# Optimization experiments

Measured on AMD Instinct MI355X. Metric: run time of the kernel, lower is better.

Reference implementation:

```python
import jax, jax.numpy as jnp
import numpy as np
from jax import lax

IMG, P, L, H, D, MLPD, NC, B = 224, 16, 12, 12, 768, 3072, 1000, 32
G = IMG // P          # 14 patches per side
S = G * G + 1         # 197 tokens (class token + patches)
DH = D // H           # 64 head dim
EPS = 1e-6


def setup_inputs() -> dict:
    key = jax.random.key(0)
    ks = jax.random.split(key, 10)
    def nrm(k, shape, s=0.02):
        return jax.random.normal(k, shape, jnp.float32) * s
    return {
        "x": jax.random.normal(ks[0], (B, 3, IMG, IMG), jnp.float32),
        "tangent": jax.random.normal(ks[1], (B, 3, IMG, IMG), jnp.float32),
        "conv_w": nrm(ks[2], (D, 3, P, P)),
        "conv_b": jnp.zeros((D,), jnp.float32),
        "class_token": jnp.zeros((1, 1, D), jnp.float32),
        "pos_emb": nrm(ks[3], (1, S, D)),
        "ln1_g": jnp.ones((L, D), jnp.float32), "ln1_b": jnp.zeros((L, D), jnp.float32),
        "qkv_w": nrm(ks[4], (L, 3 * D, D)), "qkv_b": jnp.zeros((L, 3 * D), jnp.float32),
        "out_w": nrm(ks[5], (L, D, D)), "out_b": jnp.zeros((L, D), jnp.float32),
        "ln2_g": jnp.ones((L, D), jnp.float32), "ln2_b": jnp.zeros((L, D), jnp.float32),
        "fc1_w": nrm(ks[6], (L, MLPD, D)), "fc1_b": jnp.zeros((L, MLPD), jnp.float32),
        "fc2_w": nrm(ks[7], (L, D, MLPD)), "fc2_b": jnp.zeros((L, D), jnp.float32),
        "lnf_g": jnp.ones((D,), jnp.float32), "lnf_b": jnp.zeros((D,), jnp.float32),
        "head_w": nrm(ks[8], (NC, D)), "head_b": jnp.zeros((NC,), jnp.float32),
    }


def _layer_norm(x, g, b):
    mu = jnp.mean(x, -1, keepdims=True)
    var = jnp.mean(jnp.square(x - mu), -1, keepdims=True)
    return (x - mu) * lax.rsqrt(var + EPS) * g + b


def _vit(x, conv_w, conv_b, class_token, pos_emb, ln1_g, ln1_b, qkv_w, qkv_b,
         out_w, out_b, ln2_g, ln2_b, fc1_w, fc1_b, fc2_w, fc2_b, lnf_g, lnf_b,
         head_w, head_b):
    n = x.shape[0]
    # patch embedding == Conv2d(3, D, kernel=P, stride=P)
    xr = x.reshape(n, 3, G, P, G, P)
    tok = jnp.einsum('ncgphq,dcpq->nghd', xr, conv_w).reshape(n, G * G, D) + conv_b
    cls = jnp.broadcast_to(class_token, (n, 1, D))
    z = jnp.concatenate([cls, tok], axis=1) + pos_emb  # [n, S, D]

    def block(z, p):
        l1g, l1b, qw, qb, ow, ob, l2g, l2b, f1w, f1b, f2w, f2b = p
        y = _layer_norm(z, l1g, l1b)
        qkv = jnp.einsum('nsd,ed->nse', y, qw) + qb          # [n,S,3D]
        q, k, v = jnp.split(qkv, 3, axis=-1)
        q = q.reshape(n, S, H, DH).transpose(0, 2, 1, 3)
        k = k.reshape(n, S, H, DH).transpose(0, 2, 1, 3)
        v = v.reshape(n, S, H, DH).transpose(0, 2, 1, 3)
        scores = jnp.einsum('nhqd,nhkd->nhqk', q, k) / jnp.sqrt(jnp.float32(DH))
        a = jax.nn.softmax(scores, axis=-1)
        o = jnp.einsum('nhqk,nhkd->nhqd', a, v).transpose(0, 2, 1, 3).reshape(n, S, D)
        o = jnp.einsum('nsd,ed->nse', o, ow) + ob
        z = z + o
        y2 = _layer_norm(z, l2g, l2b)
        h = jax.nn.gelu(jnp.einsum('nsd,ed->nse', y2, f1w) + f1b, approximate=False)
        z = z + jnp.einsum('nse,de->nsd', h, f2w) + f2b
        return z, None

    z, _ = lax.scan(block, z, (ln1_g, ln1_b, qkv_w, qkv_b, out_w, out_b,
                               ln2_g, ln2_b, fc1_w, fc1_b, fc2_w, fc2_b))
    z = _layer_norm(z, lnf_g, lnf_b)
    return z[:, 0] @ head_w.T + head_b  # [n, NC]


def reference(x, tangent, conv_w, conv_b, class_token, pos_emb, ln1_g, ln1_b,
              qkv_w, qkv_b, out_w, out_b, ln2_g, ln2_b, fc1_w, fc1_b, fc2_w,
              fc2_b, lnf_g, lnf_b, head_w, head_b):
    f = lambda xx: _vit(xx, conv_w, conv_b, class_token, pos_emb, ln1_g, ln1_b,
                        qkv_w, qkv_b, out_w, out_b, ln2_g, ln2_b, fc1_w, fc1_b,
                        fc2_w, fc2_b, lnf_g, lnf_b, head_w, head_b)
    out, out_jvp = jax.jvp(f, (x,), (tangent,))
    return out, out_jvp
```

## Files before the change

### kernel.cpp

```cpp
#include <hip/hip_runtime.h>
#include <math.h>

static constexpr int B_   = 32;
static constexpr int S_   = 197;
static constexpr int D_   = 768;
static constexpr int H_   = 12;
static constexpr int L_   = 12;
static constexpr int MD_  = 3072;
static constexpr int NC_  = 1000;
static constexpr int GP_  = 196;
static constexpr int KP_  = 224;
static constexpr int MP_  = 6400;

typedef __attribute__((ext_vector_type(8))) short bf16x8v;
typedef __attribute__((ext_vector_type(4))) float f32x4v;

__device__ __forceinline__ unsigned short f2bf(float x) {
    union { float f; unsigned u; } v; v.f = x;
    unsigned r = v.u + 0x7fffu + ((v.u >> 16) & 1u);
    return (unsigned short)(r >> 16);
}

#define GLOAD_LDS16(gptr, lptr) \
    __builtin_amdgcn_global_load_lds((const __attribute__((address_space(1))) void*)(gptr), \
        (__attribute__((address_space(3))) void*)(lptr), 16, 0, 0)

template<bool ACC, bool BIAS, bool OUTBF>
__global__ __launch_bounds__(512, 4) void mfma_gemm_kernel(
    const short* __restrict__ A, const short* __restrict__ Bm,
    const float* __restrict__ bias, void* __restrict__ Cv,
    int M, int N, int K, int ldc, int bias_rows)
{
    int bx, by;
    {
        const int gx = gridDim.x, nwg = gx * gridDim.y;
        const int flat = blockIdx.y * gx + blockIdx.x;
        const int q = nwg >> 3, r = nwg & 7;
        const int xcd = flat & 7, idx = flat >> 3;
        const int nf = (xcd < r ? xcd * (q + 1) : r * (q + 1) + (xcd - r) * q) + idx;
        bx = nf % gx; by = nf / gx;
    }
    __shared__ __align__(16) short ldsA[2][128 * 32];
    __shared__ __align__(16) short ldsB[2][128 * 32];
    const int tid  = threadIdx.x;
    const int lane = tid & 63;
    const int w    = tid >> 6;
    const int m0 = by * 128, n0 = bx * 128;
    const int wr = w >> 1, wc = w & 1;
    f32x4v acc[2][4] = {};

    const int r_in = lane >> 2;
    const int cdst = lane & 3;
    const int srow = w * 16 + r_in;
    const int csrc = cdst ^ ((srow >> 1) & 3);
    const size_t aoff = (size_t)(m0 + srow) * K + csrc * 8;
    const size_t boff = (size_t)(n0 + srow) * K + csrc * 8;

    GLOAD_LDS16(A  + aoff, &ldsA[0][w * 512]);
    GLOAD_LDS16(Bm + boff, &ldsB[0][w * 512]);
    __syncthreads();

    int cur = 0;
    for (int k0 = 0; k0 < K; k0 += 32) {
        const int nxt = cur ^ 1;
        if (k0 + 32 < K) {
            GLOAD_LDS16(A  + aoff + k0 + 32, &ldsA[nxt][w * 512]);
            GLOAD_LDS16(Bm + boff + k0 + 32, &ldsB[nxt][w * 512]);
        }
        const short* La = ldsA[cur];
        const short* Lb = ldsB[cur];
        bf16x8v af[2], bfr[4];
        #pragma unroll
        for (int m = 0; m < 2; ++m) {
            const int row = wr * 32 + m * 16 + (lane & 15);
            const int c = (lane >> 4) ^ ((row >> 1) & 3);
            af[m] = *(const bf16x8v*)&La[row * 32 + c * 8];
        }
        #pragma unroll
        for (int n = 0; n < 4; ++n) {
            const int row = wc * 64 + n * 16 + (lane & 15);
            const int c = (lane >> 4) ^ ((row >> 1) & 3);
            bfr[n] = *(const bf16x8v*)&Lb[row * 32 + c * 8];
        }
        #pragma unroll
        for (int m = 0; m < 2; ++m)
            #pragma unroll
            for (int n = 0; n < 4; ++n)
                acc[m][n] = __builtin_amdgcn_mfma_f32_16x16x32_bf16(af[m], bfr[n], acc[m][n], 0, 0, 0);
        __syncthreads();
        cur = nxt;
    }
    const int col_base = n0 + wc * 64 + (lane & 15);
    const int row_base = m0 + wr * 32 + (lane >> 4) * 4;
    #pragma unroll
    for (int n = 0; n < 4; ++n) {
        const int col = col_base + n * 16;
        const float bv = BIAS ? bias[col] : 0.f;
        #pragma unroll
        for (int m = 0; m < 2; ++m) {
            const int row = row_base + m * 16;
            const float bvr = (BIAS && row < bias_rows) ? bv : 0.f;
            #pragma unroll
            for (int r = 0; r < 4; ++r) {
                if (row + r < M) {
                    const size_t off = (size_t)(row + r) * ldc + col;
                    const float v = acc[m][n][r] + bvr;
                    if (OUTBF) ((short*)Cv)[off] = (short)f2bf(v);
                    else if (ACC) ((float*)Cv)[off] += v;
                    else ((float*)Cv)[off] = v;
                }
            }
        }
    }
}

__global__ __launch_bounds__(256) void attn_fused_kernel(
    const short* __restrict__ qkvb, const short* __restrict__ dqkvb,
    const short* __restrict__ Vtb_, const short* __restrict__ dVtb_,
    short* __restrict__ obf, short* __restrict__ dobf)
{
    const int qt = blockIdx.x;
    const int b  = blockIdx.y;
    const int n = b / H_, h = b - n * H_;
    const short* qb  = qkvb  + (size_t)n * S_ * 2304 + h * 64;
    const short* kb  = qb + 768;
    const short* dqb = dqkvb + (size_t)n * S_ * 2304 + h * 64;
    const short* dkb = dqb + 768;
    const short* Vb  = Vtb_  + (size_t)b * 64 * KP_;
    const short* dVb = dVtb_ + (size_t)b * 64 * KP_;

    __shared__ __align__(16) short lds[32768];
    const int tid = threadIdx.x, lane = tid & 63, w = tid >> 6;
    const int g = lane >> 4, kc = lane & 15;
    const int srow = lane >> 2, cdst = lane & 3;
    const int csrc = cdst ^ ((srow >> 1) & 3);

    {
        const size_t qr = (size_t)min(qt * 64 + w * 16 + srow, S_ - 1) * 2304;
        #pragma unroll
        for (int kw = 0; kw < 2; ++kw) {
            GLOAD_LDS16(qb  + qr + kw * 32 + csrc * 8, &lds[w * 1024 + kw * 512]);
            GLOAD_LDS16(dqb + qr + kw * 32 + csrc * 8, &lds[4096 + w * 1024 + kw * 512]);
        }
    }

    f32x4v aS[14], aD[14];
    #pragma unroll
    for (int i = 0; i < 14; ++i) { aS[i] = (f32x4v){0,0,0,0}; aD[i] = (f32x4v){0,0,0,0}; }
    bf16x8v qf[2], dqf[2];

    #pragma unroll
    for (int kt = 0; kt < 7; ++kt) {
        {
            const int kwin = w & 1;
            const short* src = (w < 2) ? kb : dkb;
            const int base = (w < 2) ? 8192 : 10240;
            #pragma unroll
            for (int half = 0; half < 2; ++half) {
                const size_t kr = (size_t)min(kt * 32 + half * 16 + srow, S_ - 1) * 2304;
                GLOAD_LDS16(src + kr + kwin * 32 + csrc * 8,
                            &lds[base + kwin * 1024 + half * 512]);
            }
        }
        __syncthreads();
        if (kt == 0) {
            #pragma unroll
            for (int kw = 0; kw < 2; ++kw) {
                const int c = g ^ ((kc >> 1) & 3);
                qf[kw]  = *(const bf16x8v*)&lds[w * 1024 + kw * 512 + kc * 32 + c * 8];
                dqf[kw] = *(const bf16x8v*)&lds[4096 + w * 1024 + kw * 512 + kc * 32 + c * 8];
            }
        }
        #pragma unroll
        for (int nf = 0; nf < 2; ++nf) {
            const int row = nf * 16 + kc;
            const int c = g ^ ((row >> 1) & 3);
            const bf16x8v kf0  = *(const bf16x8v*)&lds[8192  + row * 32 + c * 8];
            const bf16x8v kf1  = *(const bf16x8v*)&lds[8192  + 1024 + row * 32 + c * 8];
            const bf16x8v dkf0 = *(const bf16x8v*)&lds[10240 + row * 32 + c * 8];
            const bf16x8v dkf1 = *(const bf16x8v*)&lds[10240 + 1024 + row * 32 + c * 8];
            const int fi = kt * 2 + nf;
            aS[fi] = __builtin_amdgcn_mfma_f32_16x16x32_bf16(qf[0], kf0, aS[fi], 0,0,0);
            aS[fi] = __builtin_amdgcn_mfma_f32_16x16x32_bf16(qf[1], kf1, aS[fi], 0,0,0);
            aD[fi] = __builtin_amdgcn_mfma_f32_16x16x32_bf16(dqf[0], kf0, aD[fi], 0,0,0);
            aD[fi] = __builtin_amdgcn_mfma_f32_16x16x32_bf16(dqf[1], kf1, aD[fi], 0,0,0);
            aD[fi] = __builtin_amdgcn_mfma_f32_16x16x32_bf16(qf[0], dkf0, aD[fi], 0,0,0);
            aD[fi] = __builtin_amdgcn_mfma_f32_16x16x32_bf16(qf[1], dkf1, aD[fi], 0,0,0);
        }
        __syncthreads();
    }

    float pm[4] = {-3.0e38f, -3.0e38f, -3.0e38f, -3.0e38f};
    #pragma unroll
    for (int fi = 0; fi < 14; ++fi) {
        if (fi * 16 + kc < S_) {
            #pragma unroll
            for (int r = 0; r < 4; ++r) pm[r] = fmaxf(pm[r], aS[fi][r]);
        }
    }
    #pragma unroll
    for (int off = 1; off < 16; off <<= 1)
        #pragma unroll
        for (int r = 0; r < 4; ++r) pm[r] = fmaxf(pm[r], __shfl_xor(pm[r], off));

    float den[4] = {0,0,0,0}, tsm[4] = {0,0,0,0};
    #pragma unroll
    for (int fi = 0; fi < 14; ++fi) {
        const bool val = fi * 16 + kc < S_;
        #pragma unroll
        for (int r = 0; r < 4; ++r) {
            const float s  = aS[fi][r] * 0.125f;
            const float ds = aD[fi][r] * 0.125f;
            const float e = val ? expf(s - pm[r] * 0.125f) : 0.f;
            den[r] += e; tsm[r] += e * ds;
            aS[fi][r] = e; aD[fi][r] = ds;
        }
    }
    #pragma unroll
    for (int off = 1; off < 16; off <<= 1)
        #pragma unroll
        for (int r = 0; r < 4; ++r) {
            den[r] += __shfl_xor(den[r], off);
            tsm[r] += __shfl_xor(tsm[r], off);
        }
    float inv[4], tq[4];
    #pragma unroll
    for (int r = 0; r < 4; ++r) { inv[r] = 1.f / den[r]; tq[r] = tsm[r] * inv[r]; }

    const int lpw = w * 3584, ldpw = 14336 + w * 3584;
    #pragma unroll
    for (int fi = 0; fi < 14; ++fi) {
        const int kwin = fi >> 1;
        const int chunkbase = (fi & 1) * 2 + (kc >> 3);
        #pragma unroll
        for (int r = 0; r < 4; ++r) {
            const int qs = g * 4 + r;
            const int swz = chunkbase ^ ((qs >> 1) & 3);
            const int addr = kwin * 512 + qs * 32 + swz * 8 + (kc & 7);
            const float p  = aS[fi][r] * inv[r];
            const float dp = p * (aD[fi][r] - tq[r]);
            lds[lpw  + addr] = (short)f2bf(p);
            lds[ldpw + addr] = (short)f2bf(dp);
        }
    }

    f32x4v aO[4], aDO[4];
    #pragma unroll
    for (int i = 0; i < 4; ++i) { aO[i] = (f32x4v){0,0,0,0}; aDO[i] = (f32x4v){0,0,0,0}; }

    #pragma unroll
    for (int kt = 0; kt < 7; ++kt) {
        {
            const size_t vr = (size_t)(w * 16 + srow) * KP_ + kt * 32 + csrc * 8;
            GLOAD_LDS16(Vb  + vr, &lds[28672 + w * 512]);
            GLOAD_LDS16(dVb + vr, &lds[30720 + w * 512]);
        }
        __syncthreads();
        bf16x8v pa, dpa;
        {
            const int c = g ^ ((kc >> 1) & 3);
            pa  = *(const bf16x8v*)&lds[lpw  + kt * 512 + kc * 32 + c * 8];
            dpa = *(const bf16x8v*)&lds[ldpw + kt * 512 + kc * 32 + c * 8];
        }
        #pragma unroll
        for (int nf = 0; nf < 4; ++nf) {
            const int row = nf * 16 + kc;
            const int c = (g) ^ ((row >> 1) & 3);
            const bf16x8v vf  = *(const bf16x8v*)&lds[28672 + row * 32 + c * 8];
            const bf16x8v dvf = *(const bf16x8v*)&lds[30720 + row * 32 + c * 8];
            aO[nf]  = __builtin_amdgcn_mfma_f32_16x16x32_bf16(pa,  vf,  aO[nf], 0,0,0);
            aDO[nf] = __builtin_amdgcn_mfma_f32_16x16x32_bf16(dpa, vf,  aDO[nf], 0,0,0);
            aDO[nf] = __builtin_amdgcn_mfma_f32_16x16x32_bf16(pa,  dvf, aDO[nf], 0,0,0);
        }
        __syncthreads();
    }

    short* ob  = obf  + (size_t)n * S_ * D_ + h * 64;
    short* dob = dobf + (size_t)n * S_ * D_ + h * 64;
    #pragma unroll
    for (int nf = 0; nf < 4; ++nf) {
        const int dh = nf * 16 + kc;
        #pragma unroll
        for (int r = 0; r < 4; ++r) {
            const int q = qt * 64 + w * 16 + g * 4 + r;
            if (q < S_) {
                ob [(size_t)q * D_ + dh] = (short)f2bf(aO[nf][r]);
                dob[(size_t)q * D_ + dh] = (short)f2bf(aDO[nf][r]);
            }
        }
    }
}

__global__ __launch_bounds__(256) void vtrans_kernel(
    const short* __restrict__ qkvb, const short* __restrict__ dqkvb,
    short* __restrict__ Vt, short* __restrict__ dVt)
{
    const int blk = blockIdx.x;
    const int b = blk >> 2, kt = blk & 3;
    const int n = b / H_, h = b - n * H_;
    const short* vb  = qkvb  + (size_t)n * S_ * 2304 + 1536 + h * 64;
    const short* dvb = dqkvb + (size_t)n * S_ * 2304 + 1536 + h * 64;
    __shared__ short t1[64][65], t2[64][65];
    const int tid = threadIdx.x;
    #pragma unroll
    for (int j = 0; j < 16; ++j) {
        const int e = tid + 256 * j;
        const int kk = e >> 6, dh = e & 63;
        const int gk = kt * 64 + kk;
        short v = 0, dv = 0;
        if (gk < S_) { v = vb[(size_t)gk * 2304 + dh]; dv = dvb[(size_t)gk * 2304 + dh]; }
        t1[dh][kk] = v; t2[dh][kk] = dv;
    }
    __syncthreads();
    #pragma unroll
    for (int j = 0; j < 16; ++j) {
        const int e = tid + 256 * j;
        const int dh = e >> 6, kk = e & 63;
        const int ok = kt * 64 + kk;
        if (ok < KP_) {
            Vt [(size_t)b * 64 * KP_ + (size_t)dh * KP_ + ok] = t1[dh][kk];
            dVt[(size_t)b * 64 * KP_ + (size_t)dh * KP_ + ok] = t2[dh][kk];
        }
    }
}

template<bool BIAS>
__global__ __launch_bounds__(256) void gemm_kernel(
    const float* __restrict__ A, const float* __restrict__ Bm,
    const float* __restrict__ bias, float* __restrict__ C,
    int M, int N, int K, int lda, int ldb, int ldc)
{
    const int tile_m = blockIdx.y * 64, tile_n = blockIdx.x * 64;
    __shared__ float As[16][64];
    __shared__ float Bs[16][64];
    const int tid = threadIdx.x;
    const int tx = tid & 15, ty = tid >> 4;
    float acc[4][4] = {};
    for (int k0 = 0; k0 < K; k0 += 16) {
        {
            const int row = tid >> 2, kc = (tid & 3) * 4, gm = tile_m + row;
            #pragma unroll
            for (int i = 0; i < 4; ++i) {
                const int gk = k0 + kc + i;
                float v = 0.f;
                if (gm < M && gk < K) v = A[(long long)gm * lda + gk];
                As[kc + i][row] = v;
            }
        }
        {
            const int row = tid >> 2, kc = (tid & 3) * 4, gn = tile_n + row;
            #pragma unroll
            for (int i = 0; i < 4; ++i) {
                const int gk = k0 + kc + i;
                float v = 0.f;
                if (gn < N && gk < K) v = Bm[(long long)gn * ldb + gk];
                Bs[kc + i][row] = v;
            }
        }
        __syncthreads();
        #pragma unroll
        for (int kk = 0; kk < 16; ++kk) {
            float a[4], bb[4];
            #pragma unroll
            for (int i = 0; i < 4; ++i) a[i] = As[kk][ty * 4 + i];
            #pragma unroll
            for (int j = 0; j < 4; ++j) bb[j] = Bs[kk][tx * 4 + j];
            #pragma unroll
            for (int i = 0; i < 4; ++i)
                #pragma unroll
                for (int j = 0; j < 4; ++j)
                    acc[i][j] += a[i] * bb[j];
        }
        __syncthreads();
    }
    #pragma unroll
    for (int i = 0; i < 4; ++i) {
        const int gm = tile_m + ty * 4 + i;
        if (gm >= M) continue;
        #pragma unroll
        for (int j = 0; j < 4; ++j) {
            const int gn = tile_n + tx * 4 + j;
            if (gn >= N) continue;
            float v = acc[i][j];
            if (BIAS) v += bias[gn];
            C[(long long)gm * ldc + gn] = v;
        }
    }
}

__device__ __forceinline__ float blk_sum4(float v, float* smem) {
    #pragma unroll
    for (int off = 32; off > 0; off >>= 1) v += __shfl_down(v, off);
    __syncthreads();
    if ((threadIdx.x & 63) == 0) smem[threadIdx.x >> 6] = v;
    __syncthreads();
    return smem[0] + smem[1] + smem[2] + smem[3];
}

template<bool WF32>
__global__ __launch_bounds__(256) void ln_jvp_kernel(
    const float* __restrict__ z, const float* __restrict__ dz,
    const float* __restrict__ g, const float* __restrict__ b,
    float* __restrict__ y, float* __restrict__ dy,
    short* __restrict__ ybf, short* __restrict__ dybf)
{
    const long long row = blockIdx.x;
    const float* xr  = z  + row * D_;
    const float* dxr = dz + row * D_;
    __shared__ float smem[4];
    const int t = threadIdx.x;
    float x[3], dx[3];
    #pragma unroll
    for (int i = 0; i < 3; ++i) { x[i] = xr[t + 256 * i]; dx[i] = dxr[t + 256 * i]; }
    float sx  = blk_sum4(x[0] + x[1] + x[2], smem);
    float sdx = blk_sum4(dx[0] + dx[1] + dx[2], smem);
    const float mu = sx / D_, dmu = sdx / D_;
    float sv = 0.f, sc = 0.f;
    #pragma unroll
    for (int i = 0; i < 3; ++i) {
        const float xc = x[i] - mu;
        sv += xc * xc;
        sc += xc * (dx[i] - dmu);
    }
    sv = blk_sum4(sv, smem);
    sc = blk_sum4(sc, smem);
    const float rstd = rsqrtf(sv / D_ + 1e-6f);
    const float k2   = (sc / D_) * rstd * rstd;
    #pragma unroll
    for (int i = 0; i < 3; ++i) {
        const int c = t + 256 * i;
        const float yh  = (x[i] - mu) * rstd;
        const float dyh = (dx[i] - dmu) * rstd - yh * k2;
        const float yv  = yh * g[c] + b[c];
        const float dyv = dyh * g[c];
        if (WF32) { y[row * D_ + c] = yv; dy[row * D_ + c] = dyv; }
        ybf[row * D_ + c]  = (short)f2bf(yv);
        dybf[row * D_ + c] = (short)f2bf(dyv);
    }
}

__global__ __launch_bounds__(256) void gelu_jvp_kernel(
    const float* __restrict__ h, const float* __restrict__ dh,
    short* __restrict__ ho, short* __restrict__ dho, int n4)
{
    for (int i = blockIdx.x * blockDim.x + threadIdx.x; i < n4;
         i += gridDim.x * blockDim.x) {
        const float4 u4 = ((const float4*)h)[i];
        const float4 du4 = ((const float4*)dh)[i];
        short o[4], doo[4];
        const float us[4] = {u4.x, u4.y, u4.z, u4.w};
        const float dus[4] = {du4.x, du4.y, du4.z, du4.w};
        #pragma unroll
        for (int j = 0; j < 4; ++j) {
            const float u = us[j], du = dus[j];
            const float cdf = 0.5f * (1.0f + erff(u * 0.70710678118654752f));
            const float pdf = 0.3989422804014327f * expf(-0.5f * u * u);
            o[j]   = (short)f2bf(u * cdf);
            doo[j] = (short)f2bf(du * (cdf + u * pdf));
        }
        *(short4*)&ho[i * 4]  = *(short4*)o;
        *(short4*)&dho[i * 4] = *(short4*)doo;
    }
}

__global__ __launch_bounds__(256) void cast_bf16_kernel(
    const float* __restrict__ in, short* __restrict__ out, int n4)
{
    for (int i = blockIdx.x * blockDim.x + threadIdx.x; i < n4;
         i += gridDim.x * blockDim.x) {
        const float4 v = ((const float4*)in)[i];
        short o[4];
        o[0] = (short)f2bf(v.x); o[1] = (short)f2bf(v.y);
        o[2] = (short)f2bf(v.z); o[3] = (short)f2bf(v.w);
        *(short4*)&out[i * 4] = *(short4*)o;
    }
}

__global__ __launch_bounds__(256) void wcast_kernel(
    const float* __restrict__ qw, const float* __restrict__ ow,
    const float* __restrict__ f1, const float* __restrict__ f2,
    short* __restrict__ dq, short* __restrict__ dow,
    short* __restrict__ d1, short* __restrict__ d2)
{
    const int b1 = 442368;
    const int b2 = b1 + 147456;
    const int b3 = b2 + 589824;
    const int total = b3 + 589824;
    for (int i = blockIdx.x * blockDim.x + threadIdx.x; i < total;
         i += gridDim.x * blockDim.x) {
        const float* s; short* d; int j;
        if (i < b1)      { s = qw; d = dq;  j = i; }
        else if (i < b2) { s = ow; d = dow; j = i - b1; }
        else if (i < b3) { s = f1; d = d1;  j = i - b2; }
        else             { s = f2; d = d2;  j = i - b3; }
        const float4 v = ((const float4*)s)[j];
        short o[4];
        o[0] = (short)f2bf(v.x); o[1] = (short)f2bf(v.y);
        o[2] = (short)f2bf(v.z); o[3] = (short)f2bf(v.w);
        *(short4*)&d[j * 4] = *(short4*)o;
    }
}

__global__ __launch_bounds__(256) void im2col_kernel(
    const float* __restrict__ x, short* __restrict__ xp, int total)
{
    for (int i = blockIdx.x * blockDim.x + threadIdx.x; i < total;
         i += gridDim.x * blockDim.x) {
        const int k  = i % 768;
        const int m  = i / 768;
        const int gh = m % GP_;
        const int n  = m / GP_;
        const int q  = k & 15;
        const int p  = (k >> 4) & 15;
        const int c  = k >> 8;
        const int hc = gh % 14, gr = gh / 14;
        const int ir = gr * 16 + p, ic = hc * 16 + q;
        xp[i] = (short)f2bf(x[(((long long)n * 3 + c) * 224 + ir) * 224 + ic]);
    }
}

__global__ __launch_bounds__(256) void assemble_kernel(
    const float* __restrict__ tok, const float* __restrict__ dtok,
    float* __restrict__ z, float* __restrict__ dz,
    const float* __restrict__ cls, const float* __restrict__ pos, int total)
{
    for (int i = blockIdx.x * blockDim.x + threadIdx.x; i < total;
         i += gridDim.x * blockDim.x) {
        const int d = i % D_;
        const int s = (i / D_) % S_;
        const int n = i / (D_ * S_);
        if (s == 0) {
            z[i]  = cls[d] + pos[d];
            dz[i] = 0.f;
        } else {
            const long long ti = ((long long)n * GP_ + s - 1) * D_ + d;
            z[i]  = tok[ti]  + pos[s * D_ + d];
            dz[i] = dtok[ti];
        }
    }
}

static inline void mgemm(hipStream_t st, const short* A, const short* Bm, const float* bias,
                         void* C, int M, int N, int K, int ldc, int bias_rows,
                         bool acc, bool hasbias, bool outbf)
{
    dim3 grid(N / 128, (M + 127) / 128);
    dim3 blk(512);
#define MK(AC, BI, OB) mfma_gemm_kernel<AC, BI, OB><<<grid, blk, 0, st>>>(A, Bm, bias, C, M, N, K, ldc, bias_rows)
    if (outbf) { if (hasbias) MK(false, true, true); else MK(false, false, true); }
    else if (acc) { if (hasbias) MK(true, true, false);  else MK(true, false, false); }
    else     { if (hasbias) MK(false, true, false); else MK(false, false, false); }
#undef MK
}

static inline void cast_bf(hipStream_t st, const float* in, short* out, long long n) {
    const int n4 = (int)(n / 4);
    int g = (n4 + 255) / 256; if (g > 4096) g = 4096;
    cast_bf16_kernel<<<g, 256, 0, st>>>(in, out, n4);
}

extern "C" void kernel_launch(void* const* d_in, const int* in_sizes, int n_in,
                              void* d_out, int out_size, void* d_ws, size_t ws_size,
                              hipStream_t stream)
{
    const float* x       = (const float*)d_in[0];
    const float* tangent = (const float*)d_in[1];
    const float* conv_w  = (const float*)d_in[2];
    const float* conv_b  = (const float*)d_in[3];
    const float* cls     = (const float*)d_in[4];
    const float* pos     = (const float*)d_in[5];
    const float* ln1_g   = (const float*)d_in[6];
    const float* ln1_b   = (const float*)d_in[7];
    const float* qkv_w   = (const float*)d_in[8];
    const float* qkv_b   = (const float*)d_in[9];
    const float* out_w   = (const float*)d_in[10];
    const float* out_b   = (const float*)d_in[11];
    const float* ln2_g   = (const float*)d_in[12];
    const float* ln2_b   = (const float*)d_in[13];
    const float* fc1_w   = (const float*)d_in[14];
    const float* fc1_b   = (const float*)d_in[15];
    const float* fc2_w   = (const float*)d_in[16];
    const float* fc2_b   = (const float*)d_in[17];
    const float* lnf_g   = (const float*)d_in[18];
    const float* lnf_b   = (const float*)d_in[19];
    const float* head_w  = (const float*)d_in[20];
    const float* head_b  = (const float*)d_in[21];
    float* out = (float*)d_out;

    const int nBS = B_ * S_;
    const int NB = B_ * H_;
    const long long SD = (long long)S_ * D_;
    const long long PZ = (long long)MP_ * D_;
    const long long PQ = (long long)MP_ * 2304;
    const long long PH = (long long)MP_ * MD_;
    const long long PTOK = (long long)B_ * GP_ * D_;

    float* f = (float*)d_ws;
    float* z     = f;
    float* dz    = z + PZ;
    float* hbuf  = dz + PZ;
    float* dhbuf = hbuf + PH;
    float* tok   = hbuf;
    float* dtok  = hbuf + PTOK;
    float* yf    = hbuf;
    float* dyf   = dhbuf;

    short* sh     = (short*)(dhbuf + PH);
    short* ybf    = sh;
    short* dybf   = ybf + PZ;
    short* qkvbf  = dybf + PZ;
    short* dqkvbf = qkvbf + PQ;
    short* Vt     = dqkvbf + PQ;
    short* dVt    = Vt + (long long)NB * 64 * KP_;
    short* hbf    = dVt + (long long)NB * 64 * KP_;
    short* dhbf   = hbf + PH;
    short* xpbf   = hbf;
    short* dxpbf  = xpbf + PTOK;
    short* wq     = dhbf + PH;
    short* wo     = wq + 2304 * 768;
    short* w1     = wo + 768 * 768;
    short* w2     = w1 + 3072 * 768;
    short* cwbf   = w2 + 768 * 3072;

    {
        const int total = (int)PTOK;
        im2col_kernel<<<8192, 256, 0, stream>>>(x, xpbf, total);
        im2col_kernel<<<8192, 256, 0, stream>>>(tangent, dxpbf, total);
        cast_bf(stream, conv_w, cwbf, 768 * 768);
        mgemm(stream, xpbf, cwbf, conv_b, tok, 2 * B_ * GP_, D_, D_, D_,
              B_ * GP_, false, true, false);
        const int tz = (int)(B_ * SD);
        assemble_kernel<<<8192, 256, 0, stream>>>(tok, dtok, z, dz, cls, pos, tz);
    }

    for (int l = 0; l < L_; ++l) {
        const float* l1g = ln1_g + (long long)l * D_;
        const float* l1b = ln1_b + (long long)l * D_;
        const float* qb  = qkv_b + (long long)l * 3 * D_;
        const float* ob  = out_b + (long long)l * D_;
        const float* l2g = ln2_g + (long long)l * D_;
        const float* l2b = ln2_b + (long long)l * D_;
        const float* f1b = fc1_b + (long long)l * MD_;
        const float* f2b = fc2_b + (long long)l * D_;

        wcast_kernel<<<4096, 256, 0, stream>>>(
            qkv_w + (long long)l * 3 * D_ * D_, out_w + (long long)l * D_ * D_,
            fc1_w + (long long)l * MD_ * D_,    fc2_w + (long long)l * D_ * MD_,
            wq, wo, w1, w2);

        ln_jvp_kernel<false><<<nBS, 256, 0, stream>>>(z, dz, l1g, l1b, nullptr, nullptr, ybf, dybf);
        mgemm(stream, ybf, wq, qb, qkvbf, 2 * MP_, 3 * D_, D_, 3 * D_, MP_, false, true, true);

        vtrans_kernel<<<NB * 4, 256, 0, stream>>>(qkvbf, dqkvbf, Vt, dVt);
        attn_fused_kernel<<<dim3(4, NB), 256, 0, stream>>>(qkvbf, dqkvbf, Vt, dVt, ybf, dybf);

        mgemm(stream, ybf, wo, ob, z, 2 * MP_, D_, D_, D_, MP_, true, true, false);

        ln_jvp_kernel<false><<<nBS, 256, 0, stream>>>(z, dz, l2g, l2b, nullptr, nullptr, ybf, dybf);
        mgemm(stream, ybf, w1, f1b, hbuf, 2 * MP_, MD_, D_, MD_, MP_, false, true, false);
        gelu_jvp_kernel<<<4096, 256, 0, stream>>>(hbuf, dhbuf, hbf, dhbf, (int)(PH / 4));
        mgemm(stream, hbf, w2, f2b, z, 2 * MP_, D_, MD_, D_, MP_, true, true, false);
    }

    ln_jvp_kernel<true><<<nBS, 256, 0, stream>>>(z, dz, lnf_g, lnf_b, yf, dyf, ybf, dybf);
    gemm_kernel<true><<<dim3((NC_ + 63) / 64, 1), 256, 0, stream>>>(
        yf,  head_w, head_b, out,            B_, NC_, D_, (int)SD, D_, NC_);
    gemm_kernel<false><<<dim3((NC_ + 63) / 64, 1), 256, 0, stream>>>(
        dyf, head_w, nullptr, out + B_ * NC_, B_, NC_, D_, (int)SD, D_, NC_);
}
```

Measured before the change: 5.617 ms.

## Pair primal and tangent GEMMs sharing weight tiles and fuse GELU-JVP epilogue

Replaces the stacked-M GEMM with a paired kernel that loads the primal and tangent activation tiles together and reuses each weight tile for both, so two MFMA accumulator sets share one B load. The FC1 GEMM now applies GELU and its JVP in the epilogue and writes bf16 directly, which removes the fp32 hidden buffers and the separate gelu kernel. The costs are doubled accumulator registers (launch bounds occupancy cut from 4 to 2), extra LDS per block, and erf/exp evaluated inside the GEMM epilogue.

```diff
diff --git a/kernel.cpp b/kernel.cpp
--- a/kernel.cpp
+++ b/kernel.cpp
@@ -25,11 +25,12 @@
     __builtin_amdgcn_global_load_lds((const __attribute__((address_space(1))) void*)(gptr), \
         (__attribute__((address_space(3))) void*)(lptr), 16, 0, 0)
 
-template<bool ACC, bool BIAS, bool OUTBF>
-__global__ __launch_bounds__(512, 4) void mfma_gemm_kernel(
-    const short* __restrict__ A, const short* __restrict__ Bm,
-    const float* __restrict__ bias, void* __restrict__ Cv,
-    int M, int N, int K, int ldc, int bias_rows)
+template<int MODE, bool BIAS>
+__global__ __launch_bounds__(512, 2) void mfma_pair_kernel(
+    const short* __restrict__ Af, const short* __restrict__ At,
+    const short* __restrict__ Bm, const float* __restrict__ bias,
+    void* __restrict__ Cfv, void* __restrict__ Ctv,
+    int Mhalf, int N, int K, int ldc)
 {
     int bx, by;
     {
@@ -40,14 +41,15 @@
         const int nf = (xcd < r ? xcd * (q + 1) : r * (q + 1) + (xcd - r) * q) + idx;
         bx = nf % gx; by = nf / gx;
     }
-    __shared__ __align__(16) short ldsA[2][128 * 32];
-    __shared__ __align__(16) short ldsB[2][128 * 32];
+    __shared__ __align__(16) short ldsAf[2][128 * 32];
+    __shared__ __align__(16) short ldsAt[2][128 * 32];
+    __shared__ __align__(16) short ldsB [2][128 * 32];
     const int tid  = threadIdx.x;
     const int lane = tid & 63;
     const int w    = tid >> 6;
     const int m0 = by * 128, n0 = bx * 128;
     const int wr = w >> 1, wc = w & 1;
-    f32x4v acc[2][4] = {};
+    f32x4v accf[2][4] = {}, acct[2][4] = {};
 
     const int r_in = lane >> 2;
     const int cdst = lane & 3;
@@ -56,37 +58,40 @@
     const size_t aoff = (size_t)(m0 + srow) * K + csrc * 8;
     const size_t boff = (size_t)(n0 + srow) * K + csrc * 8;
 
-    GLOAD_LDS16(A  + aoff, &ldsA[0][w * 512]);
-    GLOAD_LDS16(Bm + boff, &ldsB[0][w * 512]);
+    GLOAD_LDS16(Af + aoff, &ldsAf[0][w * 512]);
+    GLOAD_LDS16(At + aoff, &ldsAt[0][w * 512]);
+    GLOAD_LDS16(Bm + boff, &ldsB [0][w * 512]);
     __syncthreads();
 
     int cur = 0;
     for (int k0 = 0; k0 < K; k0 += 32) {
         const int nxt = cur ^ 1;
         if (k0 + 32 < K) {
-            GLOAD_LDS16(A  + aoff + k0 + 32, &ldsA[nxt][w * 512]);
-            GLOAD_LDS16(Bm + boff + k0 + 32, &ldsB[nxt][w * 512]);
-        }
-        const short* La = ldsA[cur];
-        const short* Lb = ldsB[cur];
-        bf16x8v af[2], bfr[4];
+            GLOAD_LDS16(Af + aoff + k0 + 32, &ldsAf[nxt][w * 512]);
+            GLOAD_LDS16(At + aoff + k0 + 32, &ldsAt[nxt][w * 512]);
+            GLOAD_LDS16(Bm + boff + k0 + 32, &ldsB [nxt][w * 512]);
+        }
+        bf16x8v af[2], at[2], bfr[4];
         #pragma unroll
         for (int m = 0; m < 2; ++m) {
             const int row = wr * 32 + m * 16 + (lane & 15);
             const int c = (lane >> 4) ^ ((row >> 1) & 3);
-            af[m] = *(const bf16x8v*)&La[row * 32 + c * 8];
+            af[m] = *(const bf16x8v*)&ldsAf[cur][row * 32 + c * 8];
+            at[m] = *(const bf16x8v*)&ldsAt[cur][row * 32 + c * 8];
         }
         #pragma unroll
         for (int n = 0; n < 4; ++n) {
             const int row = wc * 64 + n * 16 + (lane & 15);
             const int c = (lane >> 4) ^ ((row >> 1) & 3);
-            bfr[n] = *(const bf16x8v*)&Lb[row * 32 + c * 8];
+            bfr[n] = *(const bf16x8v*)&ldsB[cur][row * 32 + c * 8];
         }
         #pragma unroll
         for (int m = 0; m < 2; ++m)
             #pragma unroll
-            for (int n = 0; n < 4; ++n)
-                acc[m][n] = __builtin_amdgcn_mfma_f32_16x16x32_bf16(af[m], bfr[n], acc[m][n], 0, 0, 0);
+            for (int n = 0; n < 4; ++n) {
+                accf[m][n] = __builtin_amdgcn_mfma_f32_16x16x32_bf16(af[m], bfr[n], accf[m][n], 0, 0, 0);
+                acct[m][n] = __builtin_amdgcn_mfma_f32_16x16x32_bf16(at[m], bfr[n], acct[m][n], 0, 0, 0);
+            }
         __syncthreads();
         cur = nxt;
     }
@@ -99,15 +104,27 @@
         #pragma unroll
         for (int m = 0; m < 2; ++m) {
             const int row = row_base + m * 16;
-            const float bvr = (BIAS && row < bias_rows) ? bv : 0.f;
             #pragma unroll
             for (int r = 0; r < 4; ++r) {
-                if (row + r < M) {
+                if (row + r < Mhalf) {
                     const size_t off = (size_t)(row + r) * ldc + col;
-                    const float v = acc[m][n][r] + bvr;
-                    if (OUTBF) ((short*)Cv)[off] = (short)f2bf(v);
-                    else if (ACC) ((float*)Cv)[off] += v;
-                    else ((float*)Cv)[off] = v;
+                    const float vf = accf[m][n][r] + bv;
+                    const float vt = acct[m][n][r];
+                    if (MODE == 0) {
+                        ((float*)Cfv)[off] = vf;
+                        ((float*)Ctv)[off] = vt;
+                    } else if (MODE == 1) {
+                        ((float*)Cfv)[off] += vf;
+                        ((float*)Ctv)[off] += vt;
+                    } else if (MODE == 2) {
+                        ((short*)Cfv)[off] = (short)f2bf(vf);
+                        ((short*)Ctv)[off] = (short)f2bf(vt);
+                    } else {
+                        const float cdf = 0.5f * (1.0f + erff(vf * 0.70710678118654752f));
+                        const float pdf = 0.3989422804014327f * expf(-0.5f * vf * vf);
+                        ((short*)Cfv)[off] = (short)f2bf(vf * cdf);
+                        ((short*)Ctv)[off] = (short)f2bf(vt * (cdf + vf * pdf));
+                    }
                 }
             }
         }
@@ -436,30 +453,6 @@
         if (WF32) { y[row * D_ + c] = yv; dy[row * D_ + c] = dyv; }
         ybf[row * D_ + c]  = (short)f2bf(yv);
         dybf[row * D_ + c] = (short)f2bf(dyv);
-    }
-}
-
-__global__ __launch_bounds__(256) void gelu_jvp_kernel(
-    const float* __restrict__ h, const float* __restrict__ dh,
-    short* __restrict__ ho, short* __restrict__ dho, int n4)
-{
-    for (int i = blockIdx.x * blockDim.x + threadIdx.x; i < n4;
-         i += gridDim.x * blockDim.x) {
-        const float4 u4 = ((const float4*)h)[i];
-        const float4 du4 = ((const float4*)dh)[i];
-        short o[4], doo[4];
-        const float us[4] = {u4.x, u4.y, u4.z, u4.w};
-        const float dus[4] = {du4.x, du4.y, du4.z, du4.w};
-        #pragma unroll
-        for (int j = 0; j < 4; ++j) {
-            const float u = us[j], du = dus[j];
-            const float cdf = 0.5f * (1.0f + erff(u * 0.70710678118654752f));
-            const float pdf = 0.3989422804014327f * expf(-0.5f * u * u);
-            o[j]   = (short)f2bf(u * cdf);
-            doo[j] = (short)f2bf(du * (cdf + u * pdf));
-        }
-        *(short4*)&ho[i * 4]  = *(short4*)o;
-        *(short4*)&dho[i * 4] = *(short4*)doo;
     }
 }
 
@@ -540,17 +533,19 @@
     }
 }
 
-static inline void mgemm(hipStream_t st, const short* A, const short* Bm, const float* bias,
-                         void* C, int M, int N, int K, int ldc, int bias_rows,
-                         bool acc, bool hasbias, bool outbf)
-{
-    dim3 grid(N / 128, (M + 127) / 128);
+static inline void mgemm_pair(hipStream_t st, const short* Af, const short* At,
+                              const short* Bm, const float* bias,
+                              void* Cf, void* Ct, int Mhalf, int N, int K, int ldc,
+                              int mode, bool hasbias)
+{
+    dim3 grid(N / 128, (Mhalf + 127) / 128);
     dim3 blk(512);
-#define MK(AC, BI, OB) mfma_gemm_kernel<AC, BI, OB><<<grid, blk, 0, st>>>(A, Bm, bias, C, M, N, K, ldc, bias_rows)
-    if (outbf) { if (hasbias) MK(false, true, true); else MK(false, false, true); }
-    else if (acc) { if (hasbias) MK(true, true, false);  else MK(true, false, false); }
-    else     { if (hasbias) MK(false, true, false); else MK(false, false, false); }
-#undef MK
+#define PK(MD_, BI) mfma_pair_kernel<MD_, BI><<<grid, blk, 0, st>>>(Af, At, Bm, bias, Cf, Ct, Mhalf, N, K, ldc)
+    if (mode == 0) { if (hasbias) PK(0, true); else PK(0, false); }
+    else if (mode == 1) { if (hasbias) PK(1, true); else PK(1, false); }
+    else if (mode == 2) { if (hasbias) PK(2, true); else PK(2, false); }
+    else { if (hasbias) PK(3, true); else PK(3, false); }
+#undef PK
 }
 
 static inline void cast_bf(hipStream_t st, const float* in, short* out, long long n) {
@@ -598,14 +593,14 @@
     float* f = (float*)d_ws;
     float* z     = f;
     float* dz    = z + PZ;
-    float* hbuf  = dz + PZ;
-    float* dhbuf = hbuf + PH;
-    float* tok   = hbuf;
-    float* dtok  = hbuf + PTOK;
-    float* yf    = hbuf;
-    float* dyf   = dhbuf;
-
-    short* sh     = (short*)(dhbuf + PH);
+    float* tok   = dz + PZ;
+    float* dtok  = tok + PTOK;
+    float* yf    = tok;
+    float* dyf   = tok + PTOK;
+    yf  = tok;
+    dyf = tok + PZ;
+
+    short* sh     = (short*)(tok + 2 * PZ);
     short* ybf    = sh;
     short* dybf   = ybf + PZ;
     short* qkvbf  = dybf + PZ;
@@ -615,7 +610,7 @@
     short* hbf    = dVt + (long long)NB * 64 * KP_;
     short* dhbf   = hbf + PH;
     short* xpbf   = hbf;
-    short* dxpbf  = xpbf + PTOK;
+    short* dxpbf  = hbf + PTOK;
     short* wq     = dhbf + PH;
     short* wo     = wq + 2304 * 768;
     short* w1     = wo + 768 * 768;
@@ -627,8 +622,8 @@
         im2col_kernel<<<8192, 256, 0, stream>>>(x, xpbf, total);
         im2col_kernel<<<8192, 256, 0, stream>>>(tangent, dxpbf, total);
         cast_bf(stream, conv_w, cwbf, 768 * 768);
-        mgemm(stream, xpbf, cwbf, conv_b, tok, 2 * B_ * GP_, D_, D_, D_,
-              B_ * GP_, false, true, false);
+        mgemm_pair(stream, xpbf, dxpbf, cwbf, conv_b, tok, dtok,
+                   B_ * GP_, D_, D_, D_, 0, true);
         const int tz = (int)(B_ * SD);
         assemble_kernel<<<8192, 256, 0, stream>>>(tok, dtok, z, dz, cls, pos, tz);
     }
@@ -649,17 +644,17 @@
             wq, wo, w1, w2);
 
         ln_jvp_kernel<false><<<nBS, 256, 0, stream>>>(z, dz, l1g, l1b, nullptr, nullptr, ybf, dybf);
-        mgemm(stream, ybf, wq, qb, qkvbf, 2 * MP_, 3 * D_, D_, 3 * D_, MP_, false, true, true);
+        mgemm_pair(stream, ybf, dybf, wq, qb, qkvbf, dqkvbf,
+                   nBS, 3 * D_, D_, 3 * D_, 2, true);
 
         vtrans_kernel<<<NB * 4, 256, 0, stream>>>(qkvbf, dqkvbf, Vt, dVt);
         attn_fused_kernel<<<dim3(4, NB), 256, 0, stream>>>(qkvbf, dqkvbf, Vt, dVt, ybf, dybf);
 
-        mgemm(stream, ybf, wo, ob, z, 2 * MP_, D_, D_, D_, MP_, true, true, false);
+        mgemm_pair(stream, ybf, dybf, wo, ob, z, dz, nBS, D_, D_, D_, 1, true);
 
         ln_jvp_kernel<false><<<nBS, 256, 0, stream>>>(z, dz, l2g, l2b, nullptr, nullptr, ybf, dybf);
-        mgemm(stream, ybf, w1, f1b, hbuf, 2 * MP_, MD_, D_, MD_, MP_, false, true, false);
-        gelu_jvp_kernel<<<4096, 256, 0, stream>>>(hbuf, dhbuf, hbf, dhbf, (int)(PH / 4));
-        mgemm(stream, hbf, w2, f2b, z, 2 * MP_, D_, MD_, D_, MP_, true, true, false);
+        mgemm_pair(stream, ybf, dybf, w1, f1b, hbf, dhbf, nBS, MD_, D_, MD_, 3, true);
+        mgemm_pair(stream, hbf, dhbf, w2, f2b, z, dz, nBS, D_, MD_, D_, 1, true);
     }
 
     ln_jvp_kernel<true><<<nBS, 256, 0, stream>>>(z, dz, lnf_g, lnf_b, yf, dyf, ybf, dybf);
```

Measured after the change: 5.081 ms. -9.5%, faster.
